# Kernel optimization log

Measured on AMD Instinct MI355X. Metric: run time of the kernel, lower is better.

## Reference

```python
import jax, jax.numpy as jnp
import numpy as np

SEQ_LEN = 4096
IN_DIM = 1024
QVK_DIM = 1024


def setup_inputs() -> dict:
    key = jax.random.key(0)
    kx, kw = jax.random.split(key)
    x = jax.random.normal(kx, (SEQ_LEN, IN_DIM), dtype=jnp.float32)
    # glorot-uniform-ish scale for W: limit = sqrt(6/(fan_in+fan_out))
    limit = np.sqrt(6.0 / (IN_DIM + 3 * QVK_DIM)).astype(np.float32)
    W = jax.random.uniform(kw, (IN_DIM, 3 * QVK_DIM), dtype=jnp.float32,
                           minval=-limit, maxval=limit)
    return {"x": x, "W": W}


def reference(x, W):
    seq_len = x.shape[0]
    qvk = x @ W                                   # [S, 3*D]
    # NOTE: original splits as queries, VALS, keys (vals is the middle chunk)
    queries, vals, keys = jnp.split(qvk, 3, axis=1)
    raw = (queries @ keys.T) / jnp.sqrt(jnp.float32(QVK_DIM))  # [S, S]
    # causal mask: strictly-upper-triangular entries -> -inf (same as the
    # original's scatter of -inf at triu_indices(seq_len, 1))
    causal = jnp.tril(jnp.ones((seq_len, seq_len), dtype=bool))
    raw = jnp.where(causal, raw, -jnp.inf)
    weights = jax.nn.softmax(raw, axis=1)
    return weights @ vals                         # [S, D]
```

## Files before the change

### kernel.cpp

```cpp
#include <hip/hip_runtime.h>

#define SEQ 4096
#define KDIM 1024
#define NQKV 3072
#define BK 32

typedef __bf16 bf16x8 __attribute__((ext_vector_type(8)));
typedef float  f32x4  __attribute__((ext_vector_type(4)));

__device__ __forceinline__ unsigned short f2b(float f) {
    unsigned int u = __float_as_uint(f);
    u += 0x7FFFu + ((u >> 16) & 1u);
    return (unsigned short)(u >> 16);
}
__device__ __forceinline__ float b2f(unsigned short h) {
    return __uint_as_float(((unsigned int)h) << 16);
}

__device__ __forceinline__ void gld_lds16(const unsigned short* g, unsigned short* l) {
    __builtin_amdgcn_global_load_lds(
        (const __attribute__((address_space(1))) void*)g,
        (__attribute__((address_space(3))) void*)l, 16, 0, 0);
}

__device__ __forceinline__ void stage_tiles(
    const unsigned short* Ag, int lda, const unsigned short* Bg, int ldb,
    int k0, unsigned short* sA, unsigned short* sB, int wave, int lane)
{
    #pragma unroll
    for (int i = 0; i < 2; ++i) {
        int c = wave * 128 + i * 64 + lane;
        int row = c >> 2, slot = c & 3;
        int p = slot ^ ((row >> 1) & 3);
        gld_lds16(Ag + row * lda + k0 + p * 8, sA + (wave * 2 + i) * 512);
        gld_lds16(Bg + row * ldb + k0 + p * 8, sB + (wave * 2 + i) * 512);
    }
}

__device__ __forceinline__ const unsigned short* frag_addr(
    const unsigned short* s, int row, int quad)
{
    return s + row * 32 + (quad ^ ((row >> 1) & 3)) * 8;
}

__device__ __forceinline__ void compute_tile(
    const unsigned short* sA, const unsigned short* sB, f32x4 acc[4][4],
    int wm, int wn, int lr, int quad)
{
    bf16x8 af[4], bq[4];
    #pragma unroll
    for (int i = 0; i < 4; ++i)
        af[i] = *(const bf16x8*)frag_addr(sA, wm + 16 * i + lr, quad);
    #pragma unroll
    for (int j = 0; j < 4; ++j)
        bq[j] = *(const bf16x8*)frag_addr(sB, wn + 16 * j + lr, quad);
    #pragma unroll
    for (int i = 0; i < 4; ++i)
        #pragma unroll
        for (int j = 0; j < 4; ++j)
            acc[i][j] = __builtin_amdgcn_mfma_f32_16x16x32_bf16(af[i], bq[j], acc[i][j], 0, 0, 0);
}

__device__ __forceinline__ void mfma_db(
    const unsigned short* Ag, int lda, const unsigned short* Bg, int ldb,
    int kLen, unsigned short* lds, f32x4 acc[4][4])
{
    const int tid  = threadIdx.x;
    const int wave = tid >> 6, lane = tid & 63;
    const int lr   = lane & 15, quad = lane >> 4;
    const int wm   = (wave >> 1) * 64, wn = (wave & 1) * 64;
    unsigned short* sA0 = lds;
    unsigned short* sB0 = lds + 4096;
    unsigned short* sA1 = lds + 8192;
    unsigned short* sB1 = lds + 12288;

    stage_tiles(Ag, lda, Bg, ldb, 0, sA0, sB0, wave, lane);
    int k = BK;
    #pragma unroll 1
    for (; k + BK < kLen; k += 2 * BK) {
        __syncthreads();
        stage_tiles(Ag, lda, Bg, ldb, k, sA1, sB1, wave, lane);
        compute_tile(sA0, sB0, acc, wm, wn, lr, quad);
        __syncthreads();
        stage_tiles(Ag, lda, Bg, ldb, k + BK, sA0, sB0, wave, lane);
        compute_tile(sA1, sB1, acc, wm, wn, lr, quad);
    }
    if (k < kLen) {
        __syncthreads();
        stage_tiles(Ag, lda, Bg, ldb, k, sA1, sB1, wave, lane);
        compute_tile(sA0, sB0, acc, wm, wn, lr, quad);
        __syncthreads();
        compute_tile(sA1, sB1, acc, wm, wn, lr, quad);
    } else {
        __syncthreads();
        compute_tile(sA0, sB0, acc, wm, wn, lr, quad);
    }
}

__device__ __forceinline__ void zero_acc(f32x4 acc[4][4]) {
    const f32x4 z = {0.f, 0.f, 0.f, 0.f};
    #pragma unroll
    for (int i = 0; i < 4; ++i)
        #pragma unroll
        for (int j = 0; j < 4; ++j) acc[i][j] = z;
}

__device__ __forceinline__ void store_rows_bf16(
    f32x4 acc[4][4], unsigned short* Cw, int ld, unsigned short* lw, int lane)
{
    const int lr = lane & 15, quad = lane >> 4;
    #pragma unroll
    for (int i = 0; i < 4; ++i) {
        #pragma unroll
        for (int j = 0; j < 4; ++j)
            #pragma unroll
            for (int r = 0; r < 4; ++r)
                lw[(quad * 4 + r) * 72 + j * 16 + lr] = f2b(acc[i][j][r]);
        #pragma unroll
        for (int t = 0; t < 2; ++t) {
            int chunk = t * 64 + lane;
            int rl = chunk >> 3, c8 = chunk & 7;
            uint4 v = *(const uint4*)(lw + rl * 72 + c8 * 8);
            *(uint4*)(Cw + (16 * i + rl) * ld + c8 * 8) = v;
        }
    }
}

__device__ __forceinline__ void store_cols_bf16(
    f32x4 acc[4][4], unsigned short* Vw, unsigned short* lw, int lane)
{
    const int lr = lane & 15, quad = lane >> 4;
    #pragma unroll
    for (int ip = 0; ip < 2; ++ip) {
        #pragma unroll
        for (int ii = 0; ii < 2; ++ii)
            #pragma unroll
            for (int j = 0; j < 4; ++j)
                #pragma unroll
                for (int r = 0; r < 4; ++r)
                    lw[(j * 16 + lr) * 40 + ii * 16 + quad * 4 + r] = f2b(acc[ip * 2 + ii][j][r]);
        #pragma unroll
        for (int t = 0; t < 4; ++t) {
            int chunk = t * 64 + lane;
            int col = chunk >> 2, c8 = chunk & 3;
            uint4 v = *(const uint4*)(lw + col * 40 + c8 * 8);
            *(uint4*)(Vw + col * SEQ + ip * 32 + c8 * 8) = v;
        }
    }
}

__global__ __launch_bounds__(256) void prep(
    const float* __restrict__ x, unsigned short* __restrict__ Xb,
    const float* __restrict__ W, unsigned short* __restrict__ Wt,
    float4* __restrict__ out, float4* __restrict__ lrow)
{
    __shared__ float tile[32][33];
    const int b = blockIdx.x, tid = threadIdx.x;
    if (b < 4096) {
        int i = (b * 256 + tid) * 4;
        float4 v = *(const float4*)(x + i);
        ushort4 o;
        o.x = f2b(v.x); o.y = f2b(v.y); o.z = f2b(v.z); o.w = f2b(v.w);
        *(ushort4*)(Xb + i) = o;
    } else if (b < 8192) {
        const float4 z = {0.f, 0.f, 0.f, 0.f};
        out[(b - 4096) * 256 + tid] = z;
    } else if (b < 11264) {
        const int bb = b - 8192;
        const int n0 = (bb % 96) * 32, k0 = (bb / 96) * 32;
        const int c = tid & 31, r0 = tid >> 5;
        #pragma unroll
        for (int r = r0; r < 32; r += 8)
            tile[r][c] = W[(k0 + r) * NQKV + n0 + c];
        __syncthreads();
        #pragma unroll
        for (int r = r0; r < 32; r += 8)
            Wt[(n0 + r) * KDIM + k0 + c] = f2b(tile[c][r]);
    } else {
        const float4 z = {0.f, 0.f, 0.f, 0.f};
        #pragma unroll
        for (int k = 0; k < 4; ++k) lrow[tid * 4 + k] = z;
    }
}

__global__ __launch_bounds__(256) void qvk_gemm(
    const unsigned short* __restrict__ Xb, const unsigned short* __restrict__ Wt,
    unsigned short* __restrict__ Qb, unsigned short* __restrict__ Kb,
    unsigned short* __restrict__ Vt)
{
    __shared__ __align__(16) unsigned short lds[16384];
    const int m0 = blockIdx.y * 128;
    const int n0 = blockIdx.x * 128;
    f32x4 acc[4][4];
    zero_acc(acc);
    mfma_db(Xb + m0 * KDIM, KDIM, Wt + n0 * KDIM, KDIM, KDIM, lds, acc);
    __syncthreads();

    const int lane = threadIdx.x & 63, wave = threadIdx.x >> 6;
    const int wm = (wave >> 1) * 64, wn = (wave & 1) * 64;
    unsigned short* lw = lds + wave * 2560;
    const int region = n0 >> 10;
    const int nloc = n0 & 1023;
    if (region == 0)
        store_rows_bf16(acc, Qb + (m0 + wm) * KDIM + nloc + wn, KDIM, lw, lane);
    else if (region == 2)
        store_rows_bf16(acc, Kb + (m0 + wm) * KDIM + nloc + wn, KDIM, lw, lane);
    else
        store_cols_bf16(acc, Vt + (nloc + wn) * SEQ + m0 + wm, lw, lane);
}

__global__ __launch_bounds__(256) void score_exp_gemm(
    const unsigned short* __restrict__ Qb, const unsigned short* __restrict__ Kb,
    unsigned short* __restrict__ Sb, float* __restrict__ lrow)
{
    __shared__ __align__(16) unsigned short lds[16384];
    const int b = blockIdx.x;
    int bm = (int)((sqrtf(8.f * (float)b + 1.f) - 1.f) * 0.5f);
    while ((bm + 1) * (bm + 2) / 2 <= b) ++bm;
    while (bm * (bm + 1) / 2 > b) --bm;
    const int bn = b - bm * (bm + 1) / 2;
    const int m0 = bm * 128, n0 = bn * 128;

    f32x4 acc[4][4];
    zero_acc(acc);
    mfma_db(Qb + m0 * KDIM, KDIM, Kb + n0 * KDIM, KDIM, KDIM, lds, acc);

    const int lane = threadIdx.x & 63, wave = threadIdx.x >> 6;
    const int lr = lane & 15, quad = lane >> 4;
    const int wm = (wave >> 1) * 64, wn = (wave & 1) * 64;
    #pragma unroll
    for (int i = 0; i < 4; ++i)
        #pragma unroll
        for (int j = 0; j < 4; ++j)
            #pragma unroll
            for (int r = 0; r < 4; ++r) {
                float v = __expf(acc[i][j][r] * 0.03125f);
                if (bm == bn) {
                    int row = wm + 16 * i + quad * 4 + r;
                    int col = wn + 16 * j + lr;
                    if (col > row) v = 0.f;
                }
                acc[i][j][r] = v;
            }
    #pragma unroll
    for (int i = 0; i < 4; ++i)
        #pragma unroll
        for (int r = 0; r < 4; ++r) {
            float s = acc[i][0][r] + acc[i][1][r] + acc[i][2][r] + acc[i][3][r];
            s += __shfl_xor(s, 1, 16);
            s += __shfl_xor(s, 2, 16);
            s += __shfl_xor(s, 4, 16);
            s += __shfl_xor(s, 8, 16);
            if (lr == 0)
                atomicAdd(&lrow[m0 + wm + 16 * i + quad * 4 + r], s);
        }
    __syncthreads();
    store_rows_bf16(acc, Sb + (m0 + wm) * SEQ + n0 + wn, SEQ, lds + wave * 2560, lane);
}

__global__ __launch_bounds__(256) void pv_gemm(
    const unsigned short* __restrict__ Sb, const unsigned short* __restrict__ Vt,
    const float* __restrict__ lrow, float* __restrict__ out)
{
    __shared__ __align__(16) unsigned short lds[16384];
    const int n0 = blockIdx.x * 128;
    const int y = blockIdx.y;
    int m, c;
    if (y < 8)       { m = y;                 c = 0; }
    else if (y < 24) { m = 8 + (y - 8) / 2;   c = (y - 8) % 2; }
    else if (y < 48) { m = 16 + (y - 24) / 3; c = (y - 24) % 3; }
    else             { m = 24 + (y - 48) / 4; c = (y - 48) % 4; }
    const int m0 = m * 128;
    const int kstart = c * 1024;
    const int kend = min((m + 1) * 128, kstart + 1024);
    const int nchunks = (m >> 3) + 1;

    f32x4 acc[4][4];
    zero_acc(acc);
    mfma_db(Sb + m0 * SEQ + kstart, SEQ, Vt + n0 * SEQ + kstart, SEQ,
            kend - kstart, lds, acc);

    const int lane = threadIdx.x & 63, wave = threadIdx.x >> 6;
    const int lr = lane & 15, quad = lane >> 4;
    const int wm = (wave >> 1) * 64, wn = (wave & 1) * 64;
    #pragma unroll
    for (int i = 0; i < 4; ++i) {
        const int rbase = m0 + wm + 16 * i + quad * 4;
        const float4 l4 = *(const float4*)(lrow + rbase);
        float inv[4] = {1.0f / l4.x, 1.0f / l4.y, 1.0f / l4.z, 1.0f / l4.w};
        #pragma unroll
        for (int j = 0; j < 4; ++j) {
            const int col = n0 + wn + 16 * j + lr;
            if (nchunks == 1) {
                #pragma unroll
                for (int r = 0; r < 4; ++r)
                    out[(rbase + r) * KDIM + col] = acc[i][j][r] * inv[r];
            } else {
                #pragma unroll
                for (int r = 0; r < 4; ++r)
                    atomicAdd(&out[(rbase + r) * KDIM + col], acc[i][j][r] * inv[r]);
            }
        }
    }
}

extern "C" void kernel_launch(void* const* d_in, const int* in_sizes, int n_in,
                              void* d_out, int out_size, void* d_ws, size_t ws_size,
                              hipStream_t stream) {
    const float* x = (const float*)d_in[0];
    const float* W = (const float*)d_in[1];
    float* out = (float*)d_out;
    char* ws = (char*)d_ws;

    unsigned short* Xb = (unsigned short*)(ws);
    unsigned short* Wt = (unsigned short*)(ws + 8388608);
    unsigned short* Qb = (unsigned short*)(ws + 14680064);
    unsigned short* Kb = (unsigned short*)(ws + 23068672);
    unsigned short* Vt = (unsigned short*)(ws + 31457280);
    unsigned short* Sb = (unsigned short*)(ws + 39845888);
    float*        lrow = (float*)(ws + 73400320);

    prep          <<<11265, 256, 0, stream>>>(x, Xb, W, Wt, (float4*)out, (float4*)lrow);
    qvk_gemm      <<<dim3(NQKV / 128, SEQ / 128), 256, 0, stream>>>(Xb, Wt, Qb, Kb, Vt);
    score_exp_gemm<<<(SEQ / 128) * (SEQ / 128 + 1) / 2, 256, 0, stream>>>(Qb, Kb, Sb, lrow);
    pv_gemm       <<<dim3(KDIM / 128, 80), 256, 0, stream>>>(Sb, Vt, lrow, out);
}
```

Measured before the change: 201.0 us.

## Replace double-buffered GEMM mainloop with 4-stage vmcnt-pipelined LDS ring and swap grid axes

The two-buffer loop with full __syncthreads is replaced by a four-slot LDS ring that keeps three K-tiles of async global-to-LDS loads in flight, waiting on partial vmcnt counts and using a raw s_barrier. The goal is to hide global load latency behind the MFMA work. Grid dimensions are transposed so consecutive blocks walk along M, which changes L2 reuse of the shared operand. The causal score kernel now launches a full 2D grid and returns early for upper-triangle blocks instead of decoding a triangular index. LDS use doubles to 64KB per block, which may cut occupancy, and the hand-written vmcnt counts depend on how many loads each stage issues.

```diff
diff --git a/kernel.cpp b/kernel.cpp
--- a/kernel.cpp
+++ b/kernel.cpp
@@ -7,6 +7,9 @@
 
 typedef __bf16 bf16x8 __attribute__((ext_vector_type(8)));
 typedef float  f32x4  __attribute__((ext_vector_type(4)));
+
+#define WAITV(n) asm volatile("s_waitcnt vmcnt(" #n ")" ::: "memory")
+#define BAR()    asm volatile("s_barrier" ::: "memory")
 
 __device__ __forceinline__ unsigned short f2b(float f) {
     unsigned int u = __float_as_uint(f);
@@ -61,7 +64,7 @@
             acc[i][j] = __builtin_amdgcn_mfma_f32_16x16x32_bf16(af[i], bq[j], acc[i][j], 0, 0, 0);
 }
 
-__device__ __forceinline__ void mfma_db(
+__device__ __forceinline__ void mfma_pipe(
     const unsigned short* Ag, int lda, const unsigned short* Bg, int ldb,
     int kLen, unsigned short* lds, f32x4 acc[4][4])
 {
@@ -69,31 +72,27 @@
     const int wave = tid >> 6, lane = tid & 63;
     const int lr   = lane & 15, quad = lane >> 4;
     const int wm   = (wave >> 1) * 64, wn = (wave & 1) * 64;
-    unsigned short* sA0 = lds;
-    unsigned short* sB0 = lds + 4096;
-    unsigned short* sA1 = lds + 8192;
-    unsigned short* sB1 = lds + 12288;
-
-    stage_tiles(Ag, lda, Bg, ldb, 0, sA0, sB0, wave, lane);
-    int k = BK;
+    const int niter = kLen >> 5;
+
+    #pragma unroll
+    for (int s = 0; s < 3; ++s)
+        if (s < niter)
+            stage_tiles(Ag, lda, Bg, ldb, s * BK,
+                        lds + s * 8192, lds + s * 8192 + 4096, wave, lane);
+
     #pragma unroll 1
-    for (; k + BK < kLen; k += 2 * BK) {
-        __syncthreads();
-        stage_tiles(Ag, lda, Bg, ldb, k, sA1, sB1, wave, lane);
-        compute_tile(sA0, sB0, acc, wm, wn, lr, quad);
-        __syncthreads();
-        stage_tiles(Ag, lda, Bg, ldb, k + BK, sA0, sB0, wave, lane);
-        compute_tile(sA1, sB1, acc, wm, wn, lr, quad);
-    }
-    if (k < kLen) {
-        __syncthreads();
-        stage_tiles(Ag, lda, Bg, ldb, k, sA1, sB1, wave, lane);
-        compute_tile(sA0, sB0, acc, wm, wn, lr, quad);
-        __syncthreads();
-        compute_tile(sA1, sB1, acc, wm, wn, lr, quad);
-    } else {
-        __syncthreads();
-        compute_tile(sA0, sB0, acc, wm, wn, lr, quad);
+    for (int k = 0; k < niter; ++k) {
+        if (k + 2 < niter)      WAITV(8);
+        else if (k + 1 < niter) WAITV(4);
+        else                    WAITV(0);
+        BAR();
+        if (k + 3 < niter) {
+            const int s = (k + 3) & 3;
+            stage_tiles(Ag, lda, Bg, ldb, (k + 3) * BK,
+                        lds + s * 8192, lds + s * 8192 + 4096, wave, lane);
+        }
+        const int c = k & 3;
+        compute_tile(lds + c * 8192, lds + c * 8192 + 4096, acc, wm, wn, lr, quad);
     }
 }
 
@@ -188,12 +187,12 @@
     unsigned short* __restrict__ Qb, unsigned short* __restrict__ Kb,
     unsigned short* __restrict__ Vt)
 {
-    __shared__ __align__(16) unsigned short lds[16384];
-    const int m0 = blockIdx.y * 128;
-    const int n0 = blockIdx.x * 128;
+    __shared__ __align__(16) unsigned short lds[32768];
+    const int m0 = blockIdx.x * 128;
+    const int n0 = blockIdx.y * 128;
     f32x4 acc[4][4];
     zero_acc(acc);
-    mfma_db(Xb + m0 * KDIM, KDIM, Wt + n0 * KDIM, KDIM, KDIM, lds, acc);
+    mfma_pipe(Xb + m0 * KDIM, KDIM, Wt + n0 * KDIM, KDIM, KDIM, lds, acc);
     __syncthreads();
 
     const int lane = threadIdx.x & 63, wave = threadIdx.x >> 6;
@@ -213,17 +212,14 @@
     const unsigned short* __restrict__ Qb, const unsigned short* __restrict__ Kb,
     unsigned short* __restrict__ Sb, float* __restrict__ lrow)
 {
-    __shared__ __align__(16) unsigned short lds[16384];
-    const int b = blockIdx.x;
-    int bm = (int)((sqrtf(8.f * (float)b + 1.f) - 1.f) * 0.5f);
-    while ((bm + 1) * (bm + 2) / 2 <= b) ++bm;
-    while (bm * (bm + 1) / 2 > b) --bm;
-    const int bn = b - bm * (bm + 1) / 2;
+    __shared__ __align__(16) unsigned short lds[32768];
+    const int bm = blockIdx.x, bn = blockIdx.y;
+    if (bn > bm) return;
     const int m0 = bm * 128, n0 = bn * 128;
 
     f32x4 acc[4][4];
     zero_acc(acc);
-    mfma_db(Qb + m0 * KDIM, KDIM, Kb + n0 * KDIM, KDIM, KDIM, lds, acc);
+    mfma_pipe(Qb + m0 * KDIM, KDIM, Kb + n0 * KDIM, KDIM, KDIM, lds, acc);
 
     const int lane = threadIdx.x & 63, wave = threadIdx.x >> 6;
     const int lr = lane & 15, quad = lane >> 4;
@@ -262,9 +258,9 @@
     const unsigned short* __restrict__ Sb, const unsigned short* __restrict__ Vt,
     const float* __restrict__ lrow, float* __restrict__ out)
 {
-    __shared__ __align__(16) unsigned short lds[16384];
-    const int n0 = blockIdx.x * 128;
-    const int y = blockIdx.y;
+    __shared__ __align__(16) unsigned short lds[32768];
+    const int n0 = blockIdx.y * 128;
+    const int y = blockIdx.x;
     int m, c;
     if (y < 8)       { m = y;                 c = 0; }
     else if (y < 24) { m = 8 + (y - 8) / 2;   c = (y - 8) % 2; }
@@ -277,8 +273,8 @@
 
     f32x4 acc[4][4];
     zero_acc(acc);
-    mfma_db(Sb + m0 * SEQ + kstart, SEQ, Vt + n0 * SEQ + kstart, SEQ,
-            kend - kstart, lds, acc);
+    mfma_pipe(Sb + m0 * SEQ + kstart, SEQ, Vt + n0 * SEQ + kstart, SEQ,
+              kend - kstart, lds, acc);
 
     const int lane = threadIdx.x & 63, wave = threadIdx.x >> 6;
     const int lr = lane & 15, quad = lane >> 4;
@@ -321,7 +317,7 @@
     float*        lrow = (float*)(ws + 73400320);
 
     prep          <<<11265, 256, 0, stream>>>(x, Xb, W, Wt, (float4*)out, (float4*)lrow);
-    qvk_gemm      <<<dim3(NQKV / 128, SEQ / 128), 256, 0, stream>>>(Xb, Wt, Qb, Kb, Vt);
-    score_exp_gemm<<<(SEQ / 128) * (SEQ / 128 + 1) / 2, 256, 0, stream>>>(Qb, Kb, Sb, lrow);
-    pv_gemm       <<<dim3(KDIM / 128, 80), 256, 0, stream>>>(Sb, Vt, lrow, out);
-}
+    qvk_gemm      <<<dim3(SEQ / 128, NQKV / 128), 256, 0, stream>>>(Xb, Wt, Qb, Kb, Vt);
+    score_exp_gemm<<<dim3(SEQ / 128, SEQ / 128), 256, 0, stream>>>(Qb, Kb, Sb, lrow);
+    pv_gemm       <<<dim3(80, KDIM / 128), 256, 0, stream>>>(Sb, Vt, lrow, out);
+}
```

New measurement: 205.5 us. 1.02x slower.

## Use triple-buffered LDS pipeline and reorder GEMM grids for L2 reuse

Applied to the files above, without the earlier changes.

Adds a three-stage LDS pipeline (mfma_pipe) with explicit vmcnt waits and a single barrier per k-step, replacing the double-buffered loop in the QVK and score GEMMs. It also swaps the grid axes so consecutive blocks share the same B tile, and replaces the triangular block-index decode with a full 2D grid whose upper-triangle blocks exit early. The deeper pipeline is meant to hide global-load latency, at the cost of more LDS per block and possibly lower occupancy. The early-exit blocks add launch overhead.

```diff
diff --git a/kernel.cpp b/kernel.cpp
--- a/kernel.cpp
+++ b/kernel.cpp
@@ -7,6 +7,9 @@
 
 typedef __bf16 bf16x8 __attribute__((ext_vector_type(8)));
 typedef float  f32x4  __attribute__((ext_vector_type(4)));
+
+#define WAITV(n) asm volatile("s_waitcnt vmcnt(" #n ")" ::: "memory")
+#define BAR()    asm volatile("s_barrier" ::: "memory")
 
 __device__ __forceinline__ unsigned short f2b(float f) {
     unsigned int u = __float_as_uint(f);
@@ -59,6 +62,37 @@
         #pragma unroll
         for (int j = 0; j < 4; ++j)
             acc[i][j] = __builtin_amdgcn_mfma_f32_16x16x32_bf16(af[i], bq[j], acc[i][j], 0, 0, 0);
+}
+
+__device__ __forceinline__ void mfma_pipe(
+    const unsigned short* Ag, int lda, const unsigned short* Bg, int ldb,
+    int kLen, unsigned short* lds, f32x4 acc[4][4])
+{
+    const int tid  = threadIdx.x;
+    const int wave = tid >> 6, lane = tid & 63;
+    const int lr   = lane & 15, quad = lane >> 4;
+    const int wm   = (wave >> 1) * 64, wn = (wave & 1) * 64;
+    const int niter = kLen >> 5;
+
+    #pragma unroll
+    for (int s = 0; s < 2; ++s)
+        if (s < niter)
+            stage_tiles(Ag, lda, Bg, ldb, s * BK,
+                        lds + s * 8192, lds + s * 8192 + 4096, wave, lane);
+
+    #pragma unroll 1
+    for (int k = 0; k < niter; ++k) {
+        if (k + 1 < niter) WAITV(4);
+        else               WAITV(0);
+        BAR();
+        if (k + 2 < niter) {
+            const int s = (k + 2) % 3;
+            stage_tiles(Ag, lda, Bg, ldb, (k + 2) * BK,
+                        lds + s * 8192, lds + s * 8192 + 4096, wave, lane);
+        }
+        const int c = k % 3;
+        compute_tile(lds + c * 8192, lds + c * 8192 + 4096, acc, wm, wn, lr, quad);
+    }
 }
 
 __device__ __forceinline__ void mfma_db(
@@ -188,12 +222,12 @@
     unsigned short* __restrict__ Qb, unsigned short* __restrict__ Kb,
     unsigned short* __restrict__ Vt)
 {
-    __shared__ __align__(16) unsigned short lds[16384];
-    const int m0 = blockIdx.y * 128;
-    const int n0 = blockIdx.x * 128;
+    __shared__ __align__(16) unsigned short lds[24576];
+    const int m0 = blockIdx.x * 128;
+    const int n0 = blockIdx.y * 128;
     f32x4 acc[4][4];
     zero_acc(acc);
-    mfma_db(Xb + m0 * KDIM, KDIM, Wt + n0 * KDIM, KDIM, KDIM, lds, acc);
+    mfma_pipe(Xb + m0 * KDIM, KDIM, Wt + n0 * KDIM, KDIM, KDIM, lds, acc);
     __syncthreads();
 
     const int lane = threadIdx.x & 63, wave = threadIdx.x >> 6;
@@ -213,17 +247,14 @@
     const unsigned short* __restrict__ Qb, const unsigned short* __restrict__ Kb,
     unsigned short* __restrict__ Sb, float* __restrict__ lrow)
 {
-    __shared__ __align__(16) unsigned short lds[16384];
-    const int b = blockIdx.x;
-    int bm = (int)((sqrtf(8.f * (float)b + 1.f) - 1.f) * 0.5f);
-    while ((bm + 1) * (bm + 2) / 2 <= b) ++bm;
-    while (bm * (bm + 1) / 2 > b) --bm;
-    const int bn = b - bm * (bm + 1) / 2;
+    __shared__ __align__(16) unsigned short lds[24576];
+    const int bm = blockIdx.x, bn = blockIdx.y;
+    if (bn > bm) return;
     const int m0 = bm * 128, n0 = bn * 128;
 
     f32x4 acc[4][4];
     zero_acc(acc);
-    mfma_db(Qb + m0 * KDIM, KDIM, Kb + n0 * KDIM, KDIM, KDIM, lds, acc);
+    mfma_pipe(Qb + m0 * KDIM, KDIM, Kb + n0 * KDIM, KDIM, KDIM, lds, acc);
 
     const int lane = threadIdx.x & 63, wave = threadIdx.x >> 6;
     const int lr = lane & 15, quad = lane >> 4;
@@ -321,7 +352,7 @@
     float*        lrow = (float*)(ws + 73400320);
 
     prep          <<<11265, 256, 0, stream>>>(x, Xb, W, Wt, (float4*)out, (float4*)lrow);
-    qvk_gemm      <<<dim3(NQKV / 128, SEQ / 128), 256, 0, stream>>>(Xb, Wt, Qb, Kb, Vt);
-    score_exp_gemm<<<(SEQ / 128) * (SEQ / 128 + 1) / 2, 256, 0, stream>>>(Qb, Kb, Sb, lrow);
+    qvk_gemm      <<<dim3(SEQ / 128, NQKV / 128), 256, 0, stream>>>(Xb, Wt, Qb, Kb, Vt);
+    score_exp_gemm<<<dim3(SEQ / 128, SEQ / 128), 256, 0, stream>>>(Qb, Kb, Sb, lrow);
     pv_gemm       <<<dim3(KDIM / 128, 80), 256, 0, stream>>>(Sb, Vt, lrow, out);
 }
```

After: 199.1 us. No clear change (-0.9%).

## Halve GEMM block tile to 64x128 across all three GEMM kernels

Applied to the files above, without the earlier changes.

Shrinks the M dimension of every MFMA block tile from 128 to 64, so each wave computes 32x64 instead of 64x64. This doubles the block count for the QKV, score and PV GEMMs, and the triangular score indexing and the PV split-K schedule are remapped to 64-row strips. It also tightens causal skipping at finer granularity and flips the qvk grid order so consecutive blocks share the W tile. The aim is better CU occupancy and load balance across the GPU. The cost is lower arithmetic intensity per block and more global loads of the B tiles.

```diff
diff --git a/kernel.cpp b/kernel.cpp
--- a/kernel.cpp
+++ b/kernel.cpp
@@ -23,16 +23,21 @@
         (__attribute__((address_space(3))) void*)l, 16, 0, 0);
 }
 
-__device__ __forceinline__ void stage_tiles(
+__device__ __forceinline__ void stage64(
     const unsigned short* Ag, int lda, const unsigned short* Bg, int ldb,
     int k0, unsigned short* sA, unsigned short* sB, int wave, int lane)
 {
+    {
+        int c = wave * 64 + lane;
+        int row = c >> 2, slot = c & 3;
+        int p = slot ^ ((row >> 1) & 3);
+        gld_lds16(Ag + row * lda + k0 + p * 8, sA + wave * 512);
+    }
     #pragma unroll
     for (int i = 0; i < 2; ++i) {
         int c = wave * 128 + i * 64 + lane;
         int row = c >> 2, slot = c & 3;
         int p = slot ^ ((row >> 1) & 3);
-        gld_lds16(Ag + row * lda + k0 + p * 8, sA + (wave * 2 + i) * 512);
         gld_lds16(Bg + row * ldb + k0 + p * 8, sB + (wave * 2 + i) * 512);
     }
 }
@@ -43,109 +48,105 @@
     return s + row * 32 + (quad ^ ((row >> 1) & 3)) * 8;
 }
 
-__device__ __forceinline__ void compute_tile(
-    const unsigned short* sA, const unsigned short* sB, f32x4 acc[4][4],
+__device__ __forceinline__ void compute64(
+    const unsigned short* sA, const unsigned short* sB, f32x4 acc[2][4],
     int wm, int wn, int lr, int quad)
 {
-    bf16x8 af[4], bq[4];
-    #pragma unroll
-    for (int i = 0; i < 4; ++i)
+    bf16x8 af[2], bq[4];
+    #pragma unroll
+    for (int i = 0; i < 2; ++i)
         af[i] = *(const bf16x8*)frag_addr(sA, wm + 16 * i + lr, quad);
     #pragma unroll
     for (int j = 0; j < 4; ++j)
         bq[j] = *(const bf16x8*)frag_addr(sB, wn + 16 * j + lr, quad);
     #pragma unroll
-    for (int i = 0; i < 4; ++i)
+    for (int i = 0; i < 2; ++i)
         #pragma unroll
         for (int j = 0; j < 4; ++j)
             acc[i][j] = __builtin_amdgcn_mfma_f32_16x16x32_bf16(af[i], bq[j], acc[i][j], 0, 0, 0);
 }
 
-__device__ __forceinline__ void mfma_db(
+__device__ __forceinline__ void mfma_db64(
     const unsigned short* Ag, int lda, const unsigned short* Bg, int ldb,
-    int kLen, unsigned short* lds, f32x4 acc[4][4])
+    int kLen, unsigned short* lds, f32x4 acc[2][4])
 {
     const int tid  = threadIdx.x;
     const int wave = tid >> 6, lane = tid & 63;
     const int lr   = lane & 15, quad = lane >> 4;
-    const int wm   = (wave >> 1) * 64, wn = (wave & 1) * 64;
+    const int wm   = (wave >> 1) * 32, wn = (wave & 1) * 64;
     unsigned short* sA0 = lds;
-    unsigned short* sB0 = lds + 4096;
-    unsigned short* sA1 = lds + 8192;
-    unsigned short* sB1 = lds + 12288;
-
-    stage_tiles(Ag, lda, Bg, ldb, 0, sA0, sB0, wave, lane);
+    unsigned short* sB0 = lds + 2048;
+    unsigned short* sA1 = lds + 6144;
+    unsigned short* sB1 = lds + 8192;
+
+    stage64(Ag, lda, Bg, ldb, 0, sA0, sB0, wave, lane);
     int k = BK;
     #pragma unroll 1
     for (; k + BK < kLen; k += 2 * BK) {
         __syncthreads();
-        stage_tiles(Ag, lda, Bg, ldb, k, sA1, sB1, wave, lane);
-        compute_tile(sA0, sB0, acc, wm, wn, lr, quad);
-        __syncthreads();
-        stage_tiles(Ag, lda, Bg, ldb, k + BK, sA0, sB0, wave, lane);
-        compute_tile(sA1, sB1, acc, wm, wn, lr, quad);
+        stage64(Ag, lda, Bg, ldb, k, sA1, sB1, wave, lane);
+        compute64(sA0, sB0, acc, wm, wn, lr, quad);
+        __syncthreads();
+        stage64(Ag, lda, Bg, ldb, k + BK, sA0, sB0, wave, lane);
+        compute64(sA1, sB1, acc, wm, wn, lr, quad);
     }
     if (k < kLen) {
         __syncthreads();
-        stage_tiles(Ag, lda, Bg, ldb, k, sA1, sB1, wave, lane);
-        compute_tile(sA0, sB0, acc, wm, wn, lr, quad);
-        __syncthreads();
-        compute_tile(sA1, sB1, acc, wm, wn, lr, quad);
+        stage64(Ag, lda, Bg, ldb, k, sA1, sB1, wave, lane);
+        compute64(sA0, sB0, acc, wm, wn, lr, quad);
+        __syncthreads();
+        compute64(sA1, sB1, acc, wm, wn, lr, quad);
     } else {
         __syncthreads();
-        compute_tile(sA0, sB0, acc, wm, wn, lr, quad);
-    }
-}
-
-__device__ __forceinline__ void zero_acc(f32x4 acc[4][4]) {
+        compute64(sA0, sB0, acc, wm, wn, lr, quad);
+    }
+}
+
+__device__ __forceinline__ void zero_acc(f32x4 acc[2][4]) {
     const f32x4 z = {0.f, 0.f, 0.f, 0.f};
     #pragma unroll
-    for (int i = 0; i < 4; ++i)
+    for (int i = 0; i < 2; ++i)
         #pragma unroll
         for (int j = 0; j < 4; ++j) acc[i][j] = z;
 }
 
-__device__ __forceinline__ void store_rows_bf16(
-    f32x4 acc[4][4], unsigned short* Cw, int ld, unsigned short* lw, int lane)
+__device__ __forceinline__ void store_rows64(
+    f32x4 acc[2][4], unsigned short* Cw, int ld, unsigned short* lw, int lane)
 {
     const int lr = lane & 15, quad = lane >> 4;
     #pragma unroll
-    for (int i = 0; i < 4; ++i) {
+    for (int i = 0; i < 2; ++i)
         #pragma unroll
         for (int j = 0; j < 4; ++j)
             #pragma unroll
             for (int r = 0; r < 4; ++r)
-                lw[(quad * 4 + r) * 72 + j * 16 + lr] = f2b(acc[i][j][r]);
-        #pragma unroll
-        for (int t = 0; t < 2; ++t) {
-            int chunk = t * 64 + lane;
-            int rl = chunk >> 3, c8 = chunk & 7;
-            uint4 v = *(const uint4*)(lw + rl * 72 + c8 * 8);
-            *(uint4*)(Cw + (16 * i + rl) * ld + c8 * 8) = v;
-        }
-    }
-}
-
-__device__ __forceinline__ void store_cols_bf16(
-    f32x4 acc[4][4], unsigned short* Vw, unsigned short* lw, int lane)
+                lw[(16 * i + quad * 4 + r) * 72 + 16 * j + lr] = f2b(acc[i][j][r]);
+    #pragma unroll
+    for (int t = 0; t < 4; ++t) {
+        int chunk = t * 64 + lane;
+        int rl = chunk >> 3, c8 = chunk & 7;
+        uint4 v = *(const uint4*)(lw + rl * 72 + c8 * 8);
+        *(uint4*)(Cw + rl * ld + c8 * 8) = v;
+    }
+}
+
+__device__ __forceinline__ void store_cols64(
+    f32x4 acc[2][4], unsigned short* Vw, unsigned short* lw, int lane)
 {
     const int lr = lane & 15, quad = lane >> 4;
     #pragma unroll
-    for (int ip = 0; ip < 2; ++ip) {
-        #pragma unroll
-        for (int ii = 0; ii < 2; ++ii)
+    for (int i = 0; i < 2; ++i)
+        #pragma unroll
+        for (int j = 0; j < 4; ++j)
             #pragma unroll
-            for (int j = 0; j < 4; ++j)
-                #pragma unroll
-                for (int r = 0; r < 4; ++r)
-                    lw[(j * 16 + lr) * 40 + ii * 16 + quad * 4 + r] = f2b(acc[ip * 2 + ii][j][r]);
-        #pragma unroll
-        for (int t = 0; t < 4; ++t) {
-            int chunk = t * 64 + lane;
-            int col = chunk >> 2, c8 = chunk & 3;
-            uint4 v = *(const uint4*)(lw + col * 40 + c8 * 8);
-            *(uint4*)(Vw + col * SEQ + ip * 32 + c8 * 8) = v;
-        }
+            for (int r = 0; r < 4; ++r)
+                lw[(16 * j + lr) * 40 + 16 * i + quad * 4 + r] = f2b(acc[i][j][r]);
+    #pragma unroll
+    for (int t = 0; t < 4; ++t) {
+        int chunk = t * 64 + lane;
+        int d = chunk >> 2, c8 = chunk & 3;
+        uint4 v = *(const uint4*)(lw + d * 40 + c8 * 8);
+        *(uint4*)(Vw + d * SEQ + c8 * 8) = v;
     }
 }
 
@@ -188,62 +189,64 @@
     unsigned short* __restrict__ Qb, unsigned short* __restrict__ Kb,
     unsigned short* __restrict__ Vt)
 {
-    __shared__ __align__(16) unsigned short lds[16384];
-    const int m0 = blockIdx.y * 128;
-    const int n0 = blockIdx.x * 128;
-    f32x4 acc[4][4];
+    __shared__ __align__(16) unsigned short lds[12288];
+    const int m0 = blockIdx.x * 64;
+    const int n0 = blockIdx.y * 128;
+    f32x4 acc[2][4];
     zero_acc(acc);
-    mfma_db(Xb + m0 * KDIM, KDIM, Wt + n0 * KDIM, KDIM, KDIM, lds, acc);
+    mfma_db64(Xb + m0 * KDIM, KDIM, Wt + n0 * KDIM, KDIM, KDIM, lds, acc);
     __syncthreads();
 
     const int lane = threadIdx.x & 63, wave = threadIdx.x >> 6;
-    const int wm = (wave >> 1) * 64, wn = (wave & 1) * 64;
-    unsigned short* lw = lds + wave * 2560;
+    const int wm = (wave >> 1) * 32, wn = (wave & 1) * 64;
     const int region = n0 >> 10;
     const int nloc = n0 & 1023;
     if (region == 0)
-        store_rows_bf16(acc, Qb + (m0 + wm) * KDIM + nloc + wn, KDIM, lw, lane);
+        store_rows64(acc, Qb + (m0 + wm) * KDIM + nloc + wn, KDIM, lds + wave * 2304, lane);
     else if (region == 2)
-        store_rows_bf16(acc, Kb + (m0 + wm) * KDIM + nloc + wn, KDIM, lw, lane);
+        store_rows64(acc, Kb + (m0 + wm) * KDIM + nloc + wn, KDIM, lds + wave * 2304, lane);
     else
-        store_cols_bf16(acc, Vt + (nloc + wn) * SEQ + m0 + wm, lw, lane);
+        store_cols64(acc, Vt + (nloc + wn) * SEQ + m0 + wm, lds + wave * 2560, lane);
 }
 
 __global__ __launch_bounds__(256) void score_exp_gemm(
     const unsigned short* __restrict__ Qb, const unsigned short* __restrict__ Kb,
     unsigned short* __restrict__ Sb, float* __restrict__ lrow)
 {
-    __shared__ __align__(16) unsigned short lds[16384];
+    __shared__ __align__(16) unsigned short lds[12288];
     const int b = blockIdx.x;
-    int bm = (int)((sqrtf(8.f * (float)b + 1.f) - 1.f) * 0.5f);
-    while ((bm + 1) * (bm + 2) / 2 <= b) ++bm;
-    while (bm * (bm + 1) / 2 > b) --bm;
-    const int bn = b - bm * (bm + 1) / 2;
-    const int m0 = bm * 128, n0 = bn * 128;
-
-    f32x4 acc[4][4];
+    int q = (int)((sqrtf(4.f * (float)b + 1.f) - 1.f) * 0.5f);
+    while ((q + 1) * (q + 2) <= b) ++q;
+    while (q * (q + 1) > b) --q;
+    const int rem = b - q * (q + 1);
+    const int mi = 2 * q + (rem > q);
+    const int bn = (rem > q) ? rem - (q + 1) : rem;
+    const int m0 = mi * 64, n0 = bn * 128;
+
+    f32x4 acc[2][4];
     zero_acc(acc);
-    mfma_db(Qb + m0 * KDIM, KDIM, Kb + n0 * KDIM, KDIM, KDIM, lds, acc);
+    mfma_db64(Qb + m0 * KDIM, KDIM, Kb + n0 * KDIM, KDIM, KDIM, lds, acc);
 
     const int lane = threadIdx.x & 63, wave = threadIdx.x >> 6;
     const int lr = lane & 15, quad = lane >> 4;
-    const int wm = (wave >> 1) * 64, wn = (wave & 1) * 64;
-    #pragma unroll
-    for (int i = 0; i < 4; ++i)
+    const int wm = (wave >> 1) * 32, wn = (wave & 1) * 64;
+    const bool diag = (bn == (mi >> 1));
+    #pragma unroll
+    for (int i = 0; i < 2; ++i)
         #pragma unroll
         for (int j = 0; j < 4; ++j)
             #pragma unroll
             for (int r = 0; r < 4; ++r) {
                 float v = __expf(acc[i][j][r] * 0.03125f);
-                if (bm == bn) {
-                    int row = wm + 16 * i + quad * 4 + r;
-                    int col = wn + 16 * j + lr;
+                if (diag) {
+                    int row = m0 + wm + 16 * i + quad * 4 + r;
+                    int col = n0 + wn + 16 * j + lr;
                     if (col > row) v = 0.f;
                 }
                 acc[i][j][r] = v;
             }
     #pragma unroll
-    for (int i = 0; i < 4; ++i)
+    for (int i = 0; i < 2; ++i)
         #pragma unroll
         for (int r = 0; r < 4; ++r) {
             float s = acc[i][0][r] + acc[i][1][r] + acc[i][2][r] + acc[i][3][r];
@@ -255,43 +258,45 @@
                 atomicAdd(&lrow[m0 + wm + 16 * i + quad * 4 + r], s);
         }
     __syncthreads();
-    store_rows_bf16(acc, Sb + (m0 + wm) * SEQ + n0 + wn, SEQ, lds + wave * 2560, lane);
+    store_rows64(acc, Sb + (m0 + wm) * SEQ + n0 + wn, SEQ, lds + wave * 2304, lane);
 }
 
 __global__ __launch_bounds__(256) void pv_gemm(
     const unsigned short* __restrict__ Sb, const unsigned short* __restrict__ Vt,
     const float* __restrict__ lrow, float* __restrict__ out)
 {
-    __shared__ __align__(16) unsigned short lds[16384];
+    __shared__ __align__(16) unsigned short lds[12288];
     const int n0 = blockIdx.x * 128;
     const int y = blockIdx.y;
-    int m, c;
-    if (y < 8)       { m = y;                 c = 0; }
-    else if (y < 24) { m = 8 + (y - 8) / 2;   c = (y - 8) % 2; }
-    else if (y < 48) { m = 16 + (y - 24) / 3; c = (y - 24) % 3; }
-    else             { m = 24 + (y - 48) / 4; c = (y - 48) % 4; }
-    const int m0 = m * 128;
+    int g, base;
+    if (y < 16)      { g = 0; base = 0; }
+    else if (y < 48) { g = 1; base = 16; }
+    else if (y < 96) { g = 2; base = 48; }
+    else             { g = 3; base = 96; }
+    const int yy = y - base;
+    const int m = 16 * g + yy / (g + 1);
+    const int c = yy % (g + 1);
+    const int m0 = m * 64;
     const int kstart = c * 1024;
-    const int kend = min((m + 1) * 128, kstart + 1024);
-    const int nchunks = (m >> 3) + 1;
-
-    f32x4 acc[4][4];
+    const int kend = min(m0 + 64, kstart + 1024);
+
+    f32x4 acc[2][4];
     zero_acc(acc);
-    mfma_db(Sb + m0 * SEQ + kstart, SEQ, Vt + n0 * SEQ + kstart, SEQ,
-            kend - kstart, lds, acc);
+    mfma_db64(Sb + m0 * SEQ + kstart, SEQ, Vt + n0 * SEQ + kstart, SEQ,
+              kend - kstart, lds, acc);
 
     const int lane = threadIdx.x & 63, wave = threadIdx.x >> 6;
     const int lr = lane & 15, quad = lane >> 4;
-    const int wm = (wave >> 1) * 64, wn = (wave & 1) * 64;
-    #pragma unroll
-    for (int i = 0; i < 4; ++i) {
+    const int wm = (wave >> 1) * 32, wn = (wave & 1) * 64;
+    #pragma unroll
+    for (int i = 0; i < 2; ++i) {
         const int rbase = m0 + wm + 16 * i + quad * 4;
         const float4 l4 = *(const float4*)(lrow + rbase);
         float inv[4] = {1.0f / l4.x, 1.0f / l4.y, 1.0f / l4.z, 1.0f / l4.w};
         #pragma unroll
         for (int j = 0; j < 4; ++j) {
             const int col = n0 + wn + 16 * j + lr;
-            if (nchunks == 1) {
+            if (g == 0) {
                 #pragma unroll
                 for (int r = 0; r < 4; ++r)
                     out[(rbase + r) * KDIM + col] = acc[i][j][r] * inv[r];
@@ -321,7 +326,7 @@
     float*        lrow = (float*)(ws + 73400320);
 
     prep          <<<11265, 256, 0, stream>>>(x, Xb, W, Wt, (float4*)out, (float4*)lrow);
-    qvk_gemm      <<<dim3(NQKV / 128, SEQ / 128), 256, 0, stream>>>(Xb, Wt, Qb, Kb, Vt);
-    score_exp_gemm<<<(SEQ / 128) * (SEQ / 128 + 1) / 2, 256, 0, stream>>>(Qb, Kb, Sb, lrow);
-    pv_gemm       <<<dim3(KDIM / 128, 80), 256, 0, stream>>>(Sb, Vt, lrow, out);
-}
+    qvk_gemm      <<<dim3(SEQ / 64, NQKV / 128), 256, 0, stream>>>(Xb, Wt, Qb, Kb, Vt);
+    score_exp_gemm<<<1056, 256, 0, stream>>>(Qb, Kb, Sb, lrow);
+    pv_gemm       <<<dim3(KDIM / 128, 160), 256, 0, stream>>>(Sb, Vt, lrow, out);
+}
```

After: 223.0 us. +11.0%, slower.
